# Kernel tuning notes

Hardware: AMD Instinct MI355X
Metric: run time of the kernel (lower is better)

The kernel has to match this reference:

```python
import jax, jax.numpy as jnp
import numpy as np

NV, C, ED, V, D, KS = 14, 2, 32, 3, 16, 3   # num_vars, codebook, embed_dim, views, depth, kernel
K_STATES = C ** NV                          # 16384 combinatorial states
B = 32


def _all_idcs():
    # itertools.product(range(C), repeat=NV) order: first variable varies slowest
    s = np.arange(K_STATES)
    pw = C ** np.arange(NV - 1, -1, -1)
    return (s[:, None] // pw[None, :]) % C  # (K, NV) int


def _convT(h, w, b):
    # torch ConvTranspose2d (stride=1, pad=0) == full conv with spatially-flipped kernel, in/out swapped
    wt = jnp.transpose(jnp.flip(w, (2, 3)), (1, 0, 2, 3))  # (out,in,k,k)
    y = jax.lax.conv_general_dilated(h, wt, (1, 1), [(KS - 1, KS - 1)] * 2,
                                     dimension_numbers=('NCHW', 'OIHW', 'NCHW'))
    return y + b[None, :, None, None]


def _decoder(z_flat, lw, lb, w1, b1, w2, b2, w3, b3):
    h = (z_flat @ lw + lb).reshape(-1, 4 * D, 1, 1)          # (K, 64, 1, 1)
    h = jax.nn.elu(_convT(h, w1, b1))                        # (K, 32, 3, 3)
    h = jax.nn.elu(_convT(h, w2, b2))                        # (K, 16, 5, 5)
    h = _convT(h, w3, b3)                                    # (K, 1, 7, 7)
    return h[:, 0]                                           # (K, 7, 7)


def setup_inputs() -> dict:
    key = jax.random.key(0)
    ks = jax.random.split(key, 6)
    sc = jnp.float32(0.05)
    return {
        'x': jax.random.normal(ks[0], (B, V, 7, 7), jnp.float32),
        'latent_embedding': jax.random.normal(ks[1], (NV, C, ED), jnp.float32),
        'lin_w': jax.random.normal(ks[2], (V, NV * ED, 4 * D), jnp.float32) * sc,
        'lin_b': jnp.zeros((V, 4 * D), jnp.float32),
        'w1': jax.random.normal(ks[3], (V, 4 * D, 2 * D, KS, KS), jnp.float32) * sc,
        'b1': jnp.zeros((V, 2 * D), jnp.float32),
        'w2': jax.random.normal(ks[4], (V, 2 * D, D, KS, KS), jnp.float32) * sc,
        'b2': jnp.zeros((V, D), jnp.float32),
        'w3': jax.random.normal(ks[5], (V, D, 1, KS, KS), jnp.float32) * sc,
        'b3': jnp.zeros((V, 1), jnp.float32),
    }


def reference(x, latent_embedding, lin_w, lin_b, w1, b1, w2, b2, w3, b3):
    idcs = jnp.asarray(_all_idcs())                                   # (K, NV) const
    z = latent_embedding[jnp.arange(NV)[None, :], idcs]               # (K, NV, ED)
    zf = z.reshape(K_STATES, NV * ED)
    means = jax.vmap(_decoder, in_axes=(None, 0, 0, 0, 0, 0, 0, 0, 0))(
        zf, lin_w, lin_b, w1, b1, w2, b2, w3, b3)                     # (V, K, 7, 7)
    means = jnp.transpose(means, (1, 0, 2, 3))                        # (K, V, 7, 7)
    # obs_logits: -0.5 * sum((means[None] - x[:, None])**2) over (h, w)
    return -0.5 * jnp.sum((means[None] - x[:, None]) ** 2, axis=(-2, -1))  # (B, K, V)
```

## Files before the change

kernel.cpp:

```cpp
#include <hip/hip_runtime.h>
#include <math.h>

#define NVARS 14
#define EDIM 32
#define VMIX 3
#define KSTATES 16384
#define BATCH 32

#define WS_DSWZ_B  32768
#define WS_W2SWZ_B (WS_DSWZ_B + 55296)
#define WS_W3SWZ_B (WS_W2SWZ_B + 718848)

#define H1S 296
#define H2S 424
#define MS  72

typedef __attribute__((ext_vector_type(8))) short bf16x8;
typedef __attribute__((ext_vector_type(4))) float f32x4;

static __device__ inline unsigned short f2bf(float f) {
    unsigned u = __float_as_uint(f);
    u += 0x7FFFu + ((u >> 16) & 1u);
    return (unsigned short)(u >> 16);
}
static __device__ inline float elu(float x) {
    return x > 0.f ? x : (__expf(x) - 1.f);
}

__global__ __launch_bounds__(256) void preA_kernel(const float* __restrict__ emb,
                                                   const float* __restrict__ lin_w,
                                                   const float* __restrict__ w2,
                                                   const float* __restrict__ w3,
                                                   float* __restrict__ ws) {
    int t = blockIdx.x * 256 + threadIdx.x;
    char* wsb = (char*)ws;
    if (t < 5376) {
        int vnc = t >> 6;
        int i = t & 63;
        int v = vnc / 28;
        int rem = vnc % 28;
        int n = rem >> 1;
        int c = rem & 1;
        const float* e = emb + (n * 2 + c) * EDIM;
        const float* lw = lin_w + ((size_t)v * 448 + n * 32) * 64 + i;
        float acc = 0.f;
        #pragma unroll
        for (int eidx = 0; eidx < 32; ++eidx)
            acc = fmaf(e[eidx], lw[eidx * 64], acc);
        ws[t] = acc;
        return;
    }
    int g = t - 5376;
    if (g >= 58368) return;
    bf16x8 o8;
    if (g < 3456) {
        #pragma unroll
        for (int j = 0; j < 8; ++j) o8[j] = 0;
    } else if (g < 48384) {
        int h = g - 3456;
        int v = h / 14976;
        int r = h % 14976;
        int kt = r / 1664;
        int r2 = r % 1664;
        int nt = r2 / 64, l = r2 % 64;
        int n = nt * 16 + (l & 15);
        int kbase = kt * 32 + ((l >> 4) & 3) * 8;
        #pragma unroll
        for (int j = 0; j < 8; ++j) {
            int k = kbase + j;
            float val = 0.f;
            if (n < 400) {
                int i = k / 9, p = k % 9;
                int py = p / 3, px = p % 3;
                int o = n / 25, q = n % 25;
                int qy = q / 5, qx = q % 5;
                int ty = qy - py, tx = qx - px;
                if (ty >= 0 && ty < 3 && tx >= 0 && tx < 3)
                    val = w2[((size_t)(v * 32 + i) * 16 + o) * 9 + ty * 3 + tx];
            }
            o8[j] = (short)f2bf(val);
        }
    } else {
        int h = g - 48384;
        int v = h / 3328;
        int r = h % 3328;
        int kt = r / 256;
        int r2 = r % 256;
        int nt = r2 / 64, l = r2 % 64;
        int n = nt * 16 + (l & 15);
        int kbase = kt * 32 + ((l >> 4) & 3) * 8;
        #pragma unroll
        for (int j = 0; j < 8; ++j) {
            int k = kbase + j;
            float val = 0.f;
            if (k < 400 && n < 49) {
                int o = k / 25, q = k % 25;
                int qy = q / 5, qx = q % 5;
                int py = n / 7, px = n % 7;
                int ty = py - qy, tx = px - qx;
                if (ty >= 0 && ty < 3 && tx >= 0 && tx < 3)
                    val = w3[(size_t)(v * 16 + o) * 9 + ty * 3 + tx];
            }
            o8[j] = (short)f2bf(val);
        }
    }
    *(bf16x8*)(wsb + WS_DSWZ_B + (size_t)g * 16) = o8;
}

__global__ __launch_bounds__(256) void preB_kernel(const float* __restrict__ lin_b,
                                                   const float* __restrict__ b1,
                                                   const float* __restrict__ w1,
                                                   const float* __restrict__ ws_ro,
                                                   float* __restrict__ ws) {
    int t = blockIdx.x * 256 + threadIdx.x;
    if (t >= VMIX * 15 * 288) return;
    int v = t / (15 * 288);
    int r = t % (15 * 288);
    int k = r / 288;
    int n = r % 288;
    const float* w1v = w1 + (size_t)v * 64 * 288;
    const float* Tv = ws_ro + (size_t)v * NVARS * 2 * 64;
    float val;
    if (k < 14) {
        const float* T0 = Tv + (k * 2 + 0) * 64;
        const float* T1 = Tv + (k * 2 + 1) * 64;
        float acc = 0.f;
        for (int i = 0; i < 64; ++i)
            acc = fmaf(T1[i] - T0[i], w1v[i * 288 + n], acc);
        val = acc;
    } else {
        const float* lbv = lin_b + v * 64;
        float acc = b1[v * 32 + n / 9];
        for (int i = 0; i < 64; ++i) {
            float u = lbv[i];
            #pragma unroll
            for (int n2 = 0; n2 < 14; ++n2)
                u += Tv[(n2 * 2 + 0) * 64 + i];
            acc = fmaf(u, w1v[i * 288 + n], acc);
        }
        val = acc;
    }
    int nt = n >> 4;
    int l = (n & 15) | ((k >> 3) << 4);
    int j = k & 7;
    unsigned short* dst = (unsigned short*)((char*)ws + WS_DSWZ_B);
    dst[((size_t)(v * 18 + nt) * 64 + l) * 8 + j] = f2bf(val);
}

__global__ __launch_bounds__(512, 4) void emission_main(const float* __restrict__ x,
                                                        const float* __restrict__ b2,
                                                        const float* __restrict__ b3p,
                                                        const float* __restrict__ ws,
                                                        float* __restrict__ out) {
    int bid = blockIdx.x;
    int group = bid / 24;
    int j24 = bid % 24;
    int v = j24 >> 3;
    int chunk = group * 8 + (j24 & 7);
    int tid = threadIdx.x;
    int w = tid >> 6;
    int l = tid & 63;
    int quad = l >> 4;
    int lc = l & 15;
    const char* wsb = (const char*)ws;

    __shared__ __align__(16) unsigned short uni[64 * H2S];
    __shared__ float sMsq[64];
    __shared__ float sXsq[32];
    __shared__ float sB2[16];

    if (tid < 16) sB2[tid] = b2[v * 16 + tid];
    if (tid < 64) sMsq[tid] = 0.f;
    if (tid >= 64 && tid < 96) {
        int b = tid - 64;
        const float* xb = x + (size_t)(b * 3 + v) * 49;
        float s = 0.f;
        #pragma unroll
        for (int p = 0; p < 49; ++p) s = fmaf(xb[p], xb[p], s);
        sXsq[b] = s;
    }

    int mt0 = w & 3;
    {
        int nh = w >> 2;
        int sg = chunk * 64 + mt0 * 16 + lc;
        bf16x8 abits;
        #pragma unroll
        for (int j = 0; j < 8; ++j) {
            int k = quad * 8 + j;
            unsigned short u = 0;
            if (k < 14) u = ((sg >> (13 - k)) & 1) ? 0x3F80 : 0;
            else if (k == 14) u = 0x3F80;
            abits[j] = (short)u;
        }
        const bf16x8* dsw = (const bf16x8*)(wsb + WS_DSWZ_B) + (size_t)v * 18 * 64;
        for (int i = 0; i < 9; ++i) {
            int nt = nh * 9 + i;
            bf16x8 bfrag = dsw[nt * 64 + l];
            f32x4 d = {0.f, 0.f, 0.f, 0.f};
            d = __builtin_amdgcn_mfma_f32_16x16x32_bf16(abits, bfrag, d, 0, 0, 0);
            #pragma unroll
            for (int r = 0; r < 4; ++r)
                uni[(mt0 * 16 + quad * 4 + r) * H1S + nt * 16 + lc] = f2bf(elu(d[r]));
        }
    }
    __syncthreads();

    int ncnt = (w < 2) ? 4 : 3;
    int n0 = (w < 2) ? 4 * w : 8 + 3 * (w - 2);
    f32x4 acc[4][4];
    #pragma unroll
    for (int mt = 0; mt < 4; ++mt)
        #pragma unroll
        for (int j = 0; j < 4; ++j)
            acc[mt][j] = (f32x4){0.f, 0.f, 0.f, 0.f};
    {
        const bf16x8* w2f = (const bf16x8*)(wsb + WS_W2SWZ_B) + (size_t)v * 9 * 26 * 64;
        for (int kt = 0; kt < 9; ++kt) {
            bf16x8 a[4];
            #pragma unroll
            for (int mt = 0; mt < 4; ++mt)
                a[mt] = *(const bf16x8*)&uni[(mt * 16 + lc) * H1S + kt * 32 + quad * 8];
            bf16x8 bfr[4];
            #pragma unroll
            for (int j = 0; j < 4; ++j)
                if (j < ncnt) bfr[j] = w2f[(kt * 26 + n0 + j) * 64 + l];
            #pragma unroll
            for (int j = 0; j < 4; ++j)
                if (j < ncnt)
                    #pragma unroll
                    for (int mt = 0; mt < 4; ++mt)
                        acc[mt][j] = __builtin_amdgcn_mfma_f32_16x16x32_bf16(a[mt], bfr[j], acc[mt][j], 0, 0, 0);
        }
    }
    __syncthreads();

    bf16x8 xf[2];
    {
        int bt = w >> 2;
        #pragma unroll
        for (int kt = 0; kt < 2; ++kt) {
            int b = bt * 16 + lc;
            #pragma unroll
            for (int j = 0; j < 8; ++j) {
                int p = kt * 32 + quad * 8 + j;
                unsigned short u = 0;
                if (p < 49) u = f2bf(x[(size_t)(b * 3 + v) * 49 + p]);
                xf[kt][j] = (short)u;
            }
        }
    }

    #pragma unroll
    for (int j = 0; j < 4; ++j) {
        if (j < ncnt) {
            int n = (n0 + j) * 16 + lc;
            #pragma unroll
            for (int mt = 0; mt < 4; ++mt) {
                #pragma unroll
                for (int r = 0; r < 4; ++r) {
                    float val = 0.f;
                    if (n < 400) {
                        int o = n / 25;
                        val = elu(acc[mt][j][r] + sB2[o]);
                    }
                    uni[(mt * 16 + quad * 4 + r) * H2S + n] = f2bf(val);
                }
            }
        }
    }
    __syncthreads();

    int ph = w >> 2;
    f32x4 acc2[2];
    acc2[0] = (f32x4){0.f, 0.f, 0.f, 0.f};
    acc2[1] = (f32x4){0.f, 0.f, 0.f, 0.f};
    {
        const bf16x8* w3f = (const bf16x8*)(wsb + WS_W3SWZ_B) + (size_t)v * 13 * 4 * 64;
        for (int kt = 0; kt < 13; ++kt) {
            bf16x8 a = *(const bf16x8*)&uni[(mt0 * 16 + lc) * H2S + kt * 32 + quad * 8];
            #pragma unroll
            for (int c = 0; c < 2; ++c) {
                int pt = ph + 2 * c;
                bf16x8 bfr = w3f[(kt * 4 + pt) * 64 + l];
                acc2[c] = __builtin_amdgcn_mfma_f32_16x16x32_bf16(a, bfr, acc2[c], 0, 0, 0);
            }
        }
    }
    float b3v = b3p[v];
    float mv[2][4];
    #pragma unroll
    for (int c = 0; c < 2; ++c) {
        int p = (ph + 2 * c) * 16 + lc;
        #pragma unroll
        for (int r = 0; r < 4; ++r)
            mv[c][r] = (p < 49) ? (acc2[c][r] + b3v) : 0.f;
    }
    #pragma unroll
    for (int r = 0; r < 4; ++r) {
        float sq = mv[0][r] * mv[0][r] + mv[1][r] * mv[1][r];
        sq += __shfl_xor(sq, 1, 64);
        sq += __shfl_xor(sq, 2, 64);
        sq += __shfl_xor(sq, 4, 64);
        sq += __shfl_xor(sq, 8, 64);
        if (lc == 0) atomicAdd(&sMsq[mt0 * 16 + quad * 4 + r], sq);
    }
    __syncthreads();
    #pragma unroll
    for (int c = 0; c < 2; ++c) {
        int p = (ph + 2 * c) * 16 + lc;
        #pragma unroll
        for (int r = 0; r < 4; ++r)
            uni[(mt0 * 16 + quad * 4 + r) * MS + p] = f2bf(mv[c][r]);
    }
    __syncthreads();

    {
        int st = w & 3, bt = w >> 2;
        f32x4 acc3 = {0.f, 0.f, 0.f, 0.f};
        #pragma unroll
        for (int kt = 0; kt < 2; ++kt) {
            bf16x8 bm = *(const bf16x8*)&uni[(st * 16 + lc) * MS + kt * 32 + quad * 8];
            acc3 = __builtin_amdgcn_mfma_f32_16x16x32_bf16(xf[kt], bm, acc3, 0, 0, 0);
        }
        int s = st * 16 + lc;
        float msq = sMsq[s];
        size_t kidx = (size_t)(chunk * 64 + s) * 3 + v;
        #pragma unroll
        for (int r = 0; r < 4; ++r) {
            int b = bt * 16 + quad * 4 + r;
            out[(size_t)b * (KSTATES * 3) + kidx] = acc3[r] - 0.5f * (msq + sXsq[b]);
        }
    }
}

extern "C" void kernel_launch(void* const* d_in, const int* in_sizes, int n_in,
                              void* d_out, int out_size, void* d_ws, size_t ws_size,
                              hipStream_t stream) {
    const float* x    = (const float*)d_in[0];
    const float* emb  = (const float*)d_in[1];
    const float* linw = (const float*)d_in[2];
    const float* linb = (const float*)d_in[3];
    const float* w1   = (const float*)d_in[4];
    const float* b1   = (const float*)d_in[5];
    const float* w2   = (const float*)d_in[6];
    const float* b2   = (const float*)d_in[7];
    const float* w3   = (const float*)d_in[8];
    const float* b3   = (const float*)d_in[9];
    float* out = (float*)d_out;
    float* ws = (float*)d_ws;

    preA_kernel<<<249, 256, 0, stream>>>(emb, linw, w2, w3, ws);
    preB_kernel<<<51, 256, 0, stream>>>(linb, b1, w1, ws, ws);
    emission_main<<<768, 512, 0, stream>>>(x, b2, b3, ws, out);
}
```

Baseline: 121.3 us.

## Merge preprocessing kernels into one launch and raise emission occupancy bound

Fuses the two preprocessing kernels into a single pre_kernel. Blocks are split by role: weight swizzling for w2/w3, per-variable difference rows of the first-layer matrix, and a bias row per view. Intermediate T values now go through shared memory instead of a global round-trip between launches. Separately, the emission kernel's launch bounds change from 4 to 6 blocks per CU and the LDS row stride H2S shrinks from 424 to 420, trading register budget and possibly bank-conflict behaviour for occupancy.

```diff
diff --git a/kernel.cpp b/kernel.cpp
--- a/kernel.cpp
+++ b/kernel.cpp
@@ -12,7 +12,7 @@
 #define WS_W3SWZ_B (WS_W2SWZ_B + 718848)
 
 #define H1S 296
-#define H2S 424
+#define H2S 420
 #define MS  72
 
 typedef __attribute__((ext_vector_type(8))) short bf16x8;
@@ -27,127 +27,154 @@
     return x > 0.f ? x : (__expf(x) - 1.f);
 }
 
-__global__ __launch_bounds__(256) void preA_kernel(const float* __restrict__ emb,
-                                                   const float* __restrict__ lin_w,
-                                                   const float* __restrict__ w2,
-                                                   const float* __restrict__ w3,
-                                                   float* __restrict__ ws) {
-    int t = blockIdx.x * 256 + threadIdx.x;
+__global__ __launch_bounds__(320) void pre_kernel(const float* __restrict__ emb,
+                                                  const float* __restrict__ lin_w,
+                                                  const float* __restrict__ lin_b,
+                                                  const float* __restrict__ b1,
+                                                  const float* __restrict__ w1,
+                                                  const float* __restrict__ w2,
+                                                  const float* __restrict__ w3,
+                                                  float* __restrict__ ws) {
+    int blk = blockIdx.x;
+    int tid = threadIdx.x;
     char* wsb = (char*)ws;
-    if (t < 5376) {
-        int vnc = t >> 6;
-        int i = t & 63;
-        int v = vnc / 28;
-        int rem = vnc % 28;
-        int n = rem >> 1;
-        int c = rem & 1;
-        const float* e = emb + (n * 2 + c) * EDIM;
-        const float* lw = lin_w + ((size_t)v * 448 + n * 32) * 64 + i;
-        float acc = 0.f;
-        #pragma unroll
-        for (int eidx = 0; eidx < 32; ++eidx)
-            acc = fmaf(e[eidx], lw[eidx * 64], acc);
-        ws[t] = acc;
+    unsigned short* dmat = (unsigned short*)(wsb + WS_DSWZ_B);
+    __shared__ float sP[128];
+    __shared__ float sQ[64];
+
+    if (blk < 172) {
+        int g2 = blk * 320 + tid;
+        if (g2 >= 54912) return;
+        bf16x8 o8;
+        if (g2 < 44928) {
+            int h = g2;
+            int v = h / 14976;
+            int r = h % 14976;
+            int kt = r / 1664;
+            int r2 = r % 1664;
+            int nt = r2 / 64, l = r2 % 64;
+            int n = nt * 16 + (l & 15);
+            int kbase = kt * 32 + ((l >> 4) & 3) * 8;
+            #pragma unroll
+            for (int j = 0; j < 8; ++j) {
+                int k = kbase + j;
+                float val = 0.f;
+                if (n < 400) {
+                    int i = k / 9, p = k % 9;
+                    int py = p / 3, px = p % 3;
+                    int o = n / 25, q = n % 25;
+                    int qy = q / 5, qx = q % 5;
+                    int ty = qy - py, tx = qx - px;
+                    if (ty >= 0 && ty < 3 && tx >= 0 && tx < 3)
+                        val = w2[((size_t)(v * 32 + i) * 16 + o) * 9 + ty * 3 + tx];
+                }
+                o8[j] = (short)f2bf(val);
+            }
+        } else {
+            int h = g2 - 44928;
+            int v = h / 3328;
+            int r = h % 3328;
+            int kt = r / 256;
+            int r2 = r % 256;
+            int nt = r2 / 64, l = r2 % 64;
+            int n = nt * 16 + (l & 15);
+            int kbase = kt * 32 + ((l >> 4) & 3) * 8;
+            #pragma unroll
+            for (int j = 0; j < 8; ++j) {
+                int k = kbase + j;
+                float val = 0.f;
+                if (k < 400 && n < 49) {
+                    int o = k / 25, q = k % 25;
+                    int qy = q / 5, qx = q % 5;
+                    int py = n / 7, px = n % 7;
+                    int ty = py - qy, tx = px - qx;
+                    if (ty >= 0 && ty < 3 && tx >= 0 && tx < 3)
+                        val = w3[(size_t)(v * 16 + o) * 9 + ty * 3 + tx];
+                }
+                o8[j] = (short)f2bf(val);
+            }
+        }
+        *(bf16x8*)(wsb + WS_DSWZ_B + ((size_t)g2 + 3456) * 16) = o8;
         return;
     }
-    int g = t - 5376;
-    if (g >= 58368) return;
-    bf16x8 o8;
-    if (g < 3456) {
-        #pragma unroll
-        for (int j = 0; j < 8; ++j) o8[j] = 0;
-    } else if (g < 48384) {
-        int h = g - 3456;
-        int v = h / 14976;
-        int r = h % 14976;
-        int kt = r / 1664;
-        int r2 = r % 1664;
-        int nt = r2 / 64, l = r2 % 64;
-        int n = nt * 16 + (l & 15);
-        int kbase = kt * 32 + ((l >> 4) & 3) * 8;
-        #pragma unroll
-        for (int j = 0; j < 8; ++j) {
-            int k = kbase + j;
-            float val = 0.f;
-            if (n < 400) {
-                int i = k / 9, p = k % 9;
-                int py = p / 3, px = p % 3;
-                int o = n / 25, q = n % 25;
-                int qy = q / 5, qx = q % 5;
-                int ty = qy - py, tx = qx - px;
-                if (ty >= 0 && ty < 3 && tx >= 0 && tx < 3)
-                    val = w2[((size_t)(v * 32 + i) * 16 + o) * 9 + ty * 3 + tx];
-            }
-            o8[j] = (short)f2bf(val);
-        }
-    } else {
-        int h = g - 48384;
-        int v = h / 3328;
-        int r = h % 3328;
-        int kt = r / 256;
-        int r2 = r % 256;
-        int nt = r2 / 64, l = r2 % 64;
-        int n = nt * 16 + (l & 15);
-        int kbase = kt * 32 + ((l >> 4) & 3) * 8;
-        #pragma unroll
-        for (int j = 0; j < 8; ++j) {
-            int k = kbase + j;
-            float val = 0.f;
-            if (k < 400 && n < 49) {
-                int o = k / 25, q = k % 25;
-                int qy = q / 5, qx = q % 5;
-                int py = n / 7, px = n % 7;
-                int ty = py - qy, tx = px - qx;
-                if (ty >= 0 && ty < 3 && tx >= 0 && tx < 3)
-                    val = w3[(size_t)(v * 16 + o) * 9 + ty * 3 + tx];
-            }
-            o8[j] = (short)f2bf(val);
-        }
-    }
-    *(bf16x8*)(wsb + WS_DSWZ_B + (size_t)g * 16) = o8;
-}
-
-__global__ __launch_bounds__(256) void preB_kernel(const float* __restrict__ lin_b,
-                                                   const float* __restrict__ b1,
-                                                   const float* __restrict__ w1,
-                                                   const float* __restrict__ ws_ro,
-                                                   float* __restrict__ ws) {
-    int t = blockIdx.x * 256 + threadIdx.x;
-    if (t >= VMIX * 15 * 288) return;
-    int v = t / (15 * 288);
-    int r = t % (15 * 288);
-    int k = r / 288;
-    int n = r % 288;
-    const float* w1v = w1 + (size_t)v * 64 * 288;
-    const float* Tv = ws_ro + (size_t)v * NVARS * 2 * 64;
-    float val;
-    if (k < 14) {
-        const float* T0 = Tv + (k * 2 + 0) * 64;
-        const float* T1 = Tv + (k * 2 + 1) * 64;
-        float acc = 0.f;
-        for (int i = 0; i < 64; ++i)
-            acc = fmaf(T1[i] - T0[i], w1v[i * 288 + n], acc);
-        val = acc;
-    } else {
-        const float* lbv = lin_b + v * 64;
-        float acc = b1[v * 32 + n / 9];
-        for (int i = 0; i < 64; ++i) {
-            float u = lbv[i];
-            #pragma unroll
-            for (int n2 = 0; n2 < 14; ++n2)
-                u += Tv[(n2 * 2 + 0) * 64 + i];
-            acc = fmaf(u, w1v[i * 288 + n], acc);
-        }
-        val = acc;
-    }
-    int nt = n >> 4;
-    int l = (n & 15) | ((k >> 3) << 4);
-    int j = k & 7;
-    unsigned short* dst = (unsigned short*)((char*)ws + WS_DSWZ_B);
-    dst[((size_t)(v * 18 + nt) * 64 + l) * 8 + j] = f2bf(val);
-}
-
-__global__ __launch_bounds__(512, 4) void emission_main(const float* __restrict__ x,
+
+    if (blk < 214) {
+        int b = blk - 172;
+        int v = b / 14;
+        int k = b % 14;
+        if (tid < 128) {
+            int c = tid >> 6, i = tid & 63;
+            const float* e = emb + (k * 2 + c) * EDIM;
+            const float* lw = lin_w + ((size_t)v * 448 + k * 32) * 64 + i;
+            float a0 = 0.f, a1 = 0.f;
+            #pragma unroll
+            for (int e2 = 0; e2 < 32; e2 += 2) {
+                a0 = fmaf(e[e2], lw[e2 * 64], a0);
+                a1 = fmaf(e[e2 + 1], lw[(e2 + 1) * 64], a1);
+            }
+            sP[tid] = a0 + a1;
+        }
+        __syncthreads();
+        if (tid < 64) sQ[tid] = sP[64 + tid] - sP[tid];
+        __syncthreads();
+        if (tid < 288) {
+            int n = tid;
+            const float* w1v = w1 + (size_t)v * 64 * 288 + n;
+            float a0 = 0.f, a1 = 0.f;
+            #pragma unroll
+            for (int i = 0; i < 64; i += 2) {
+                a0 = fmaf(sQ[i], w1v[i * 288], a0);
+                a1 = fmaf(sQ[i + 1], w1v[(i + 1) * 288], a1);
+            }
+            int nt = n >> 4;
+            int l = (n & 15) | ((k >> 3) << 4);
+            dmat[((size_t)(v * 18 + nt) * 64 + l) * 8 + (k & 7)] = f2bf(a0 + a1);
+        }
+        return;
+    }
+
+    {
+        int v = blk - 214;
+        for (int t = tid; t < 9216; t += 320) {
+            int j3 = t & 7;
+            int l = (t >> 3) & 63;
+            int k2 = ((l >> 4) << 3) | j3;
+            if (k2 >= 15) dmat[(size_t)v * 9216 + t] = 0;
+        }
+        if (tid < 128) {
+            int half = tid >> 6, i = tid & 63;
+            float a0 = 0.f, a1 = 0.f;
+            for (int n2 = half * 7; n2 < half * 7 + 7; ++n2) {
+                const float* e = emb + (n2 * 2) * EDIM;
+                const float* lw = lin_w + ((size_t)v * 448 + n2 * 32) * 64 + i;
+                #pragma unroll
+                for (int e2 = 0; e2 < 32; e2 += 2) {
+                    a0 = fmaf(e[e2], lw[e2 * 64], a0);
+                    a1 = fmaf(e[e2 + 1], lw[(e2 + 1) * 64], a1);
+                }
+            }
+            sP[tid] = a0 + a1;
+        }
+        __syncthreads();
+        if (tid < 64) sQ[tid] = lin_b[v * 64 + tid] + sP[tid] + sP[64 + tid];
+        __syncthreads();
+        if (tid < 288) {
+            int n = tid;
+            const float* w1v = w1 + (size_t)v * 64 * 288 + n;
+            float a0 = b1[v * 32 + n / 9], a1 = 0.f;
+            #pragma unroll
+            for (int i = 0; i < 64; i += 2) {
+                a0 = fmaf(sQ[i], w1v[i * 288], a0);
+                a1 = fmaf(sQ[i + 1], w1v[(i + 1) * 288], a1);
+            }
+            int nt = n >> 4;
+            int l = (n & 15) | 16;
+            dmat[((size_t)(v * 18 + nt) * 64 + l) * 8 + 6] = f2bf(a0 + a1);
+        }
+    }
+}
+
+__global__ __launch_bounds__(512, 6) void emission_main(const float* __restrict__ x,
                                                         const float* __restrict__ b2,
                                                         const float* __restrict__ b3p,
                                                         const float* __restrict__ ws,
@@ -350,7 +377,6 @@
     float* out = (float*)d_out;
     float* ws = (float*)d_ws;
 
-    preA_kernel<<<249, 256, 0, stream>>>(emb, linw, w2, w3, ws);
-    preB_kernel<<<51, 256, 0, stream>>>(linb, b1, w1, ws, ws);
+    pre_kernel<<<217, 320, 0, stream>>>(emb, linw, linb, b1, w1, w2, w3, ws);
     emission_main<<<768, 512, 0, stream>>>(x, b2, b3, ws, out);
 }
```

After: 164.8 us. 35.8% more time.
